# Kernel tuning notes

Hardware: AMD Instinct MI355X
Metric: run time of the kernel (lower is better)

Reference implementation:

```python
import jax, jax.numpy as jnp
import numpy as np

TEMPERATURE = 1.0
EPS = 1e-5
COS_EPS = 1e-8  # torch CosineSimilarity default eps
N_POS, N_NEG, D = 512, 512, 512


def setup_inputs() -> dict:
    key = jax.random.key(0)
    k1, k2, k3 = jax.random.split(key, 3)
    tensor_positive = jax.random.normal(k1, (N_POS, D), dtype=jnp.float32)
    tensor_negative = jax.random.normal(k2, (N_NEG, D), dtype=jnp.float32)
    # nn.Linear(512*3, 1), weight ~ N(0, 0.02^2), bias zeros
    linear_w = jax.random.normal(k3, (1, 3 * D), dtype=jnp.float32) * 0.02
    linear_b = jnp.zeros((1,), dtype=jnp.float32)
    return {"tensor_positive": tensor_positive, "tensor_negative": tensor_negative,
            "linear_w": linear_w, "linear_b": linear_b}


def _cos_matrix(a, b):
    # pairwise cosine similarity [Na, Nb], matching torch CosineSimilarity eps clamp
    an = a / jnp.maximum(jnp.linalg.norm(a, axis=-1, keepdims=True), COS_EPS)
    bn = b / jnp.maximum(jnp.linalg.norm(b, axis=-1, keepdims=True), COS_EPS)
    return an @ bn.T


def reference(tensor_positive, tensor_negative, linear_w, linear_b):
    pos, neg = tensor_positive, tensor_negative
    n_pos, d = pos.shape
    n_neg = neg.shape[0]

    # NCE part
    logit_n = jnp.exp(_cos_matrix(pos, neg) / TEMPERATURE)        # [N, M]
    deno_n = jnp.sum(logit_n, axis=-1)                            # [N]
    logit_p = jnp.exp(_cos_matrix(pos, pos) / TEMPERATURE)        # [N, N]
    loss = jnp.sum(-jnp.log(logit_p / (deno_n[:, None] + logit_p + EPS)))

    # Pairwise classifier: linear(cat([a, b, |a-b|])) decomposed as
    # a@w1 + b@w2 + |a-b|@w3 to avoid materializing the 3D concat.
    w = linear_w[0]
    w1, w2, w3 = w[:d], w[d:2 * d], w[2 * d:]
    allv = jnp.concatenate([pos, neg], axis=0)                    # [N+M, D]
    t1 = pos @ w1                                                 # [N]
    t2 = allv @ w2                                                # [N+M]
    diff = jnp.abs(pos[:, None, :] - allv[None, :, :])            # [N, N+M, D]
    t3 = jnp.einsum('nmd,d->nm', diff, w3)                        # [N, N+M]
    logits = t1[:, None] + t2[None, :] + t3 + linear_b[0]
    labels = jnp.concatenate([jnp.ones((n_pos,), jnp.float32),
                              jnp.zeros((n_neg,), jnp.float32)])  # [N+M]
    # BCE(sigmoid(logits), labels), stable form; per-i mean then sum over i
    bce = labels[None, :] * jax.nn.softplus(-logits) + (1.0 - labels[None, :]) * jax.nn.softplus(logits)
    loss = loss + jnp.sum(jnp.mean(bce, axis=1))
    return loss
```

## Files before the change

### kernel.cpp

```cpp
#include <hip/hip_runtime.h>
#include <math.h>

#define NPOS 512
#define DIM  512
#define NB   1024
#define EPSV 1e-5f
#define COS_EPS 1e-8f

#define OFF_INV  0
#define OFF_T1   1024
#define OFF_T2   1536
#define OFF_DENO 2560
#define OFF_COS  3072

__device__ __forceinline__ float softplus_f(float x) {
    return fmaxf(x, 0.f) + __logf(1.f + __expf(-fabsf(x)));
}

__global__ __launch_bounds__(256) void prep_kernel(
    const float* __restrict__ pos, const float* __restrict__ neg,
    const float* __restrict__ w, float* __restrict__ ws, float* __restrict__ out)
{
    int gtid = blockIdx.x * 256 + threadIdx.x;
    if (gtid == 0) out[0] = 0.f;
    if (gtid < NPOS) ws[OFF_DENO + gtid] = 0.f;
    int row  = gtid >> 6;
    int lane = threadIdx.x & 63;
    if (row >= NB) return;
    bool is_pos = row < NPOS;
    const float* r = is_pos ? pos + row * DIM : neg + (row - NPOS) * DIM;

    const float4* r4  = (const float4*)r + lane * 2;
    const float4* w14 = (const float4*)(w) + lane * 2;
    const float4* w24 = (const float4*)(w + DIM) + lane * 2;
    float4 a0 = r4[0],  a1 = r4[1];
    float4 u0 = w14[0], u1 = w14[1];
    float4 v0 = w24[0], v1 = w24[1];

    float ss  = a0.x*a0.x + a0.y*a0.y + a0.z*a0.z + a0.w*a0.w
              + a1.x*a1.x + a1.y*a1.y + a1.z*a1.z + a1.w*a1.w;
    float dw1 = a0.x*u0.x + a0.y*u0.y + a0.z*u0.z + a0.w*u0.w
              + a1.x*u1.x + a1.y*u1.y + a1.z*u1.z + a1.w*u1.w;
    float dw2 = a0.x*v0.x + a0.y*v0.y + a0.z*v0.z + a0.w*v0.w
              + a1.x*v1.x + a1.y*v1.y + a1.z*v1.z + a1.w*v1.w;

    #pragma unroll
    for (int off = 32; off; off >>= 1) {
        ss  += __shfl_xor(ss, off);
        dw1 += __shfl_xor(dw1, off);
        dw2 += __shfl_xor(dw2, off);
    }
    if (lane == 0) {
        float inv = 1.f / fmaxf(sqrtf(ss), COS_EPS);
        ws[OFF_INV + row] = inv;
        ws[OFF_T2 + row]  = dw2;
        if (is_pos) ws[OFF_T1 + row] = dw1;
    }
}

__global__ __launch_bounds__(256) void fused_kernel(
    const float* __restrict__ pos, const float* __restrict__ neg,
    const float* __restrict__ w, const float* __restrict__ lb,
    float* __restrict__ ws, float* __restrict__ out)
{
    __shared__ __align__(16) float As[2][32][36];
    __shared__ __align__(16) float Bs[2][32][36];
    __shared__ float red[4];

    const int tid = threadIdx.x;
    const int n0 = blockIdx.y * 32;
    const int m0 = blockIdx.x * 32;
    const bool isneg = (m0 >= NPOS);
    const float* Asrc = pos + (size_t)n0 * DIM;
    const float* Bsrc = isneg ? (neg + (size_t)(m0 - NPOS) * DIM)
                              : (pos + (size_t)m0 * DIM);
    const float* w3 = w + 2 * DIM;

    const int lr = tid >> 3;
    const int lc = (tid & 7) << 2;
    const int ti = tid >> 4;
    const int tj = tid & 15;

    float c[2][2] = {{0.f}}, t[2][2] = {{0.f}};

    float4 a0 = *(const float4*)(Asrc + lr * DIM + lc);
    float4 b0 = *(const float4*)(Bsrc + lr * DIM + lc);
    *(float4*)&As[0][lr][lc] = a0;
    *(float4*)&Bs[0][lr][lc] = b0;
    __syncthreads();

    #pragma unroll 1
    for (int iter = 0; iter < DIM / 32; ++iter) {
        const int cur = iter & 1;
        const bool more = (iter < DIM / 32 - 1);
        if (more) {
            const float* ap = Asrc + (iter + 1) * 32;
            const float* bp = Bsrc + (iter + 1) * 32;
            a0 = *(const float4*)(ap + lr * DIM + lc);
            b0 = *(const float4*)(bp + lr * DIM + lc);
        }
        const float* w3i = w3 + iter * 32;
        #pragma unroll
        for (int k = 0; k < 32; k += 4) {
            float4 av0 = *(const float4*)&As[cur][ti][k];
            float4 av1 = *(const float4*)&As[cur][ti + 16][k];
            float4 bv0 = *(const float4*)&Bs[cur][tj][k];
            float4 bv1 = *(const float4*)&Bs[cur][tj + 16][k];
            const float4 wv = *(const float4*)(w3i + k);
            #define ACC(r, s, AV, BV) \
                c[r][s] = fmaf(AV.x, BV.x, c[r][s]); \
                c[r][s] = fmaf(AV.y, BV.y, c[r][s]); \
                c[r][s] = fmaf(AV.z, BV.z, c[r][s]); \
                c[r][s] = fmaf(AV.w, BV.w, c[r][s]); \
                t[r][s] = fmaf(fabsf(AV.x - BV.x), wv.x, t[r][s]); \
                t[r][s] = fmaf(fabsf(AV.y - BV.y), wv.y, t[r][s]); \
                t[r][s] = fmaf(fabsf(AV.z - BV.z), wv.z, t[r][s]); \
                t[r][s] = fmaf(fabsf(AV.w - BV.w), wv.w, t[r][s]);
            ACC(0, 0, av0, bv0)
            ACC(0, 1, av0, bv1)
            ACC(1, 0, av1, bv0)
            ACC(1, 1, av1, bv1)
            #undef ACC
        }
        if (more) {
            *(float4*)&As[cur ^ 1][lr][lc] = a0;
            *(float4*)&Bs[cur ^ 1][lr][lc] = b0;
            __syncthreads();
        }
    }

    const float bias = lb[0];
    float inv_n[2], t1_n[2], inv_m[2], t2_m[2];
    #pragma unroll
    for (int r = 0; r < 2; ++r) {
        int n = n0 + ti + 16 * r;
        inv_n[r] = ws[OFF_INV + n];
        t1_n[r]  = ws[OFF_T1 + n];
    }
    #pragma unroll
    for (int s = 0; s < 2; ++s) {
        int m = m0 + tj + 16 * s;
        inv_m[s] = ws[OFF_INV + m];
        t2_m[s]  = ws[OFF_T2 + m];
    }

    float bce = 0.f;
    float rowsum[2] = {0.f, 0.f};
    #pragma unroll
    for (int r = 0; r < 2; ++r) {
        #pragma unroll
        for (int s = 0; s < 2; ++s) {
            float cc = c[r][s] * inv_n[r] * inv_m[s];
            float lg = t1_n[r] + t2_m[s] + t[r][s] + bias;
            bce += softplus_f(isneg ? lg : -lg);
            if (isneg) {
                rowsum[r] += __expf(cc);
            } else {
                int n = n0 + ti + 16 * r;
                int m = m0 + tj + 16 * s;
                ws[OFF_COS + (size_t)n * NPOS + m] = cc;
            }
        }
    }

    if (isneg) {
        #pragma unroll
        for (int off = 1; off < 16; off <<= 1) {
            rowsum[0] += __shfl_xor(rowsum[0], off);
            rowsum[1] += __shfl_xor(rowsum[1], off);
        }
        if (tj == 0) {
            atomicAdd(&ws[OFF_DENO + n0 + ti], rowsum[0]);
            atomicAdd(&ws[OFF_DENO + n0 + ti + 16], rowsum[1]);
        }
    }

    #pragma unroll
    for (int off = 32; off; off >>= 1) bce += __shfl_xor(bce, off);
    const int lane = tid & 63, wid = tid >> 6;
    if (lane == 0) red[wid] = bce;
    __syncthreads();
    if (tid == 0)
        atomicAdd(out, (red[0] + red[1] + red[2] + red[3]) * (1.f / 1024.f));
}

__global__ __launch_bounds__(128) void finish_kernel(
    float* __restrict__ ws, float* __restrict__ out)
{
    const int n = blockIdx.x * 2 + (threadIdx.x >> 6);
    const int l = threadIdx.x & 63;
    const float4* C = (const float4*)(ws + OFF_COS + (size_t)n * NPOS);
    const float deno = ws[OFF_DENO + n];

    float part = 0.f;
    #pragma unroll
    for (int j = 0; j < 2; ++j) {
        float4 cc = C[l + 64 * j];
        part += __logf(deno + __expf(cc.x) + EPSV) - cc.x;
        part += __logf(deno + __expf(cc.y) + EPSV) - cc.y;
        part += __logf(deno + __expf(cc.z) + EPSV) - cc.z;
        part += __logf(deno + __expf(cc.w) + EPSV) - cc.w;
    }

    #pragma unroll
    for (int off = 32; off; off >>= 1) part += __shfl_xor(part, off);
    if (l == 0) atomicAdd(out, part);
}

extern "C" void kernel_launch(void* const* d_in, const int* in_sizes, int n_in,
                              void* d_out, int out_size, void* d_ws, size_t ws_size,
                              hipStream_t stream) {
    (void)in_sizes; (void)n_in; (void)out_size; (void)ws_size;
    const float* pos = (const float*)d_in[0];
    const float* neg = (const float*)d_in[1];
    const float* w   = (const float*)d_in[2];
    const float* lb  = (const float*)d_in[3];
    float* out = (float*)d_out;
    float* ws  = (float*)d_ws;

    prep_kernel<<<256, 256, 0, stream>>>(pos, neg, w, ws, out);
    fused_kernel<<<dim3(32, 16), 256, 0, stream>>>(pos, neg, w, lb, ws, out);
    finish_kernel<<<256, 128, 0, stream>>>(ws, out);
}
```

Measured before the change: 99.04 us.

## Fold norm/projection prep into main tile kernel and replace atomics with partial buffers

New measurement: 113.4 us. 1.15x slower.

```diff
diff --git a/kernel.cpp b/kernel.cpp
--- a/kernel.cpp
+++ b/kernel.cpp
@@ -7,84 +7,54 @@
 #define EPSV 1e-5f
 #define COS_EPS 1e-8f
 
-#define OFF_INV  0
-#define OFF_T1   1024
-#define OFF_T2   1536
-#define OFF_DENO 2560
-#define OFF_COS  3072
+#define OFF_COS   0
+#define OFF_DENOP (NPOS * NPOS)
+#define OFF_BCEP  (OFF_DENOP + 16 * NPOS)
 
 __device__ __forceinline__ float softplus_f(float x) {
     return fmaxf(x, 0.f) + __logf(1.f + __expf(-fabsf(x)));
 }
 
-__global__ __launch_bounds__(256) void prep_kernel(
-    const float* __restrict__ pos, const float* __restrict__ neg,
-    const float* __restrict__ w, float* __restrict__ ws, float* __restrict__ out)
-{
-    int gtid = blockIdx.x * 256 + threadIdx.x;
-    if (gtid == 0) out[0] = 0.f;
-    if (gtid < NPOS) ws[OFF_DENO + gtid] = 0.f;
-    int row  = gtid >> 6;
-    int lane = threadIdx.x & 63;
-    if (row >= NB) return;
-    bool is_pos = row < NPOS;
-    const float* r = is_pos ? pos + row * DIM : neg + (row - NPOS) * DIM;
-
-    const float4* r4  = (const float4*)r + lane * 2;
-    const float4* w14 = (const float4*)(w) + lane * 2;
-    const float4* w24 = (const float4*)(w + DIM) + lane * 2;
-    float4 a0 = r4[0],  a1 = r4[1];
-    float4 u0 = w14[0], u1 = w14[1];
-    float4 v0 = w24[0], v1 = w24[1];
-
-    float ss  = a0.x*a0.x + a0.y*a0.y + a0.z*a0.z + a0.w*a0.w
-              + a1.x*a1.x + a1.y*a1.y + a1.z*a1.z + a1.w*a1.w;
-    float dw1 = a0.x*u0.x + a0.y*u0.y + a0.z*u0.z + a0.w*u0.w
-              + a1.x*u1.x + a1.y*u1.y + a1.z*u1.z + a1.w*u1.w;
-    float dw2 = a0.x*v0.x + a0.y*v0.y + a0.z*v0.z + a0.w*v0.w
-              + a1.x*v1.x + a1.y*v1.y + a1.z*v1.z + a1.w*v1.w;
-
-    #pragma unroll
-    for (int off = 32; off; off >>= 1) {
-        ss  += __shfl_xor(ss, off);
-        dw1 += __shfl_xor(dw1, off);
-        dw2 += __shfl_xor(dw2, off);
-    }
-    if (lane == 0) {
-        float inv = 1.f / fmaxf(sqrtf(ss), COS_EPS);
-        ws[OFF_INV + row] = inv;
-        ws[OFF_T2 + row]  = dw2;
-        if (is_pos) ws[OFF_T1 + row] = dw1;
-    }
-}
-
-__global__ __launch_bounds__(256) void fused_kernel(
+__device__ __forceinline__ float dot4(float4 a, float4 b) {
+    return a.x * b.x + a.y * b.y + a.z * b.z + a.w * b.w;
+}
+
+__global__ __launch_bounds__(256) void mega_kernel(
     const float* __restrict__ pos, const float* __restrict__ neg,
     const float* __restrict__ w, const float* __restrict__ lb,
     float* __restrict__ ws, float* __restrict__ out)
 {
     __shared__ __align__(16) float As[2][32][36];
     __shared__ __align__(16) float Bs[2][32][36];
+    __shared__ float smInvA[32], smT1A[32], smInvB[32], smT2B[32];
     __shared__ float red[4];
 
     const int tid = threadIdx.x;
     const int n0 = blockIdx.y * 32;
     const int m0 = blockIdx.x * 32;
+    const int bid = blockIdx.y * 32 + blockIdx.x;
     const bool isneg = (m0 >= NPOS);
     const float* Asrc = pos + (size_t)n0 * DIM;
     const float* Bsrc = isneg ? (neg + (size_t)(m0 - NPOS) * DIM)
                               : (pos + (size_t)m0 * DIM);
     const float* w3 = w + 2 * DIM;
 
+    if (bid == 0 && tid == 0) out[0] = 0.f;
+
     const int lr = tid >> 3;
     const int lc = (tid & 7) << 2;
     const int ti = tid >> 4;
     const int tj = tid & 15;
 
     float c[2][2] = {{0.f}}, t[2][2] = {{0.f}};
+    float ssa = 0.f, ssb = 0.f, t1a = 0.f, t2b = 0.f;
 
     float4 a0 = *(const float4*)(Asrc + lr * DIM + lc);
     float4 b0 = *(const float4*)(Bsrc + lr * DIM + lc);
+    float4 w1c = *(const float4*)(w + lc);
+    float4 w2c = *(const float4*)(w + DIM + lc);
+    ssa += dot4(a0, a0);  t1a += dot4(a0, w1c);
+    ssb += dot4(b0, b0);  t2b += dot4(b0, w2c);
     *(float4*)&As[0][lr][lc] = a0;
     *(float4*)&Bs[0][lr][lc] = b0;
     __syncthreads();
@@ -96,8 +66,10 @@
         if (more) {
             const float* ap = Asrc + (iter + 1) * 32;
             const float* bp = Bsrc + (iter + 1) * 32;
-            a0 = *(const float4*)(ap + lr * DIM + lc);
-            b0 = *(const float4*)(bp + lr * DIM + lc);
+            a0  = *(const float4*)(ap + lr * DIM + lc);
+            b0  = *(const float4*)(bp + lr * DIM + lc);
+            w1c = *(const float4*)(w + (iter + 1) * 32 + lc);
+            w2c = *(const float4*)(w + DIM + (iter + 1) * 32 + lc);
         }
         const float* w3i = w3 + iter * 32;
         #pragma unroll
@@ -123,25 +95,40 @@
             #undef ACC
         }
         if (more) {
+            ssa += dot4(a0, a0);  t1a += dot4(a0, w1c);
+            ssb += dot4(b0, b0);  t2b += dot4(b0, w2c);
             *(float4*)&As[cur ^ 1][lr][lc] = a0;
             *(float4*)&Bs[cur ^ 1][lr][lc] = b0;
             __syncthreads();
         }
     }
 
+    #pragma unroll
+    for (int off = 1; off < 8; off <<= 1) {
+        ssa += __shfl_xor(ssa, off);
+        t1a += __shfl_xor(t1a, off);
+        ssb += __shfl_xor(ssb, off);
+        t2b += __shfl_xor(t2b, off);
+    }
+    if ((tid & 7) == 0) {
+        smInvA[lr] = 1.f / fmaxf(sqrtf(ssa), COS_EPS);
+        smT1A[lr]  = t1a;
+        smInvB[lr] = 1.f / fmaxf(sqrtf(ssb), COS_EPS);
+        smT2B[lr]  = t2b;
+    }
+    __syncthreads();
+
     const float bias = lb[0];
     float inv_n[2], t1_n[2], inv_m[2], t2_m[2];
     #pragma unroll
     for (int r = 0; r < 2; ++r) {
-        int n = n0 + ti + 16 * r;
-        inv_n[r] = ws[OFF_INV + n];
-        t1_n[r]  = ws[OFF_T1 + n];
+        inv_n[r] = smInvA[ti + 16 * r];
+        t1_n[r]  = smT1A[ti + 16 * r];
     }
     #pragma unroll
     for (int s = 0; s < 2; ++s) {
-        int m = m0 + tj + 16 * s;
-        inv_m[s] = ws[OFF_INV + m];
-        t2_m[s]  = ws[OFF_T2 + m];
+        inv_m[s] = smInvB[tj + 16 * s];
+        t2_m[s]  = smT2B[tj + 16 * s];
     }
 
     float bce = 0.f;
@@ -169,9 +156,10 @@
             rowsum[0] += __shfl_xor(rowsum[0], off);
             rowsum[1] += __shfl_xor(rowsum[1], off);
         }
+        const int mb = blockIdx.x - 16;
         if (tj == 0) {
-            atomicAdd(&ws[OFF_DENO + n0 + ti], rowsum[0]);
-            atomicAdd(&ws[OFF_DENO + n0 + ti + 16], rowsum[1]);
+            ws[OFF_DENOP + mb * NPOS + n0 + ti]      = rowsum[0];
+            ws[OFF_DENOP + mb * NPOS + n0 + ti + 16] = rowsum[1];
         }
     }
 
@@ -181,30 +169,34 @@
     if (lane == 0) red[wid] = bce;
     __syncthreads();
     if (tid == 0)
-        atomicAdd(out, (red[0] + red[1] + red[2] + red[3]) * (1.f / 1024.f));
-}
-
-__global__ __launch_bounds__(128) void finish_kernel(
+        ws[OFF_BCEP + bid] = red[0] + red[1] + red[2] + red[3];
+}
+
+__global__ __launch_bounds__(256) void finish_kernel(
     float* __restrict__ ws, float* __restrict__ out)
 {
-    const int n = blockIdx.x * 2 + (threadIdx.x >> 6);
-    const int l = threadIdx.x & 63;
-    const float4* C = (const float4*)(ws + OFF_COS + (size_t)n * NPOS);
-    const float deno = ws[OFF_DENO + n];
-
-    float part = 0.f;
-    #pragma unroll
-    for (int j = 0; j < 2; ++j) {
-        float4 cc = C[l + 64 * j];
-        part += __logf(deno + __expf(cc.x) + EPSV) - cc.x;
-        part += __logf(deno + __expf(cc.y) + EPSV) - cc.y;
-        part += __logf(deno + __expf(cc.z) + EPSV) - cc.z;
-        part += __logf(deno + __expf(cc.w) + EPSV) - cc.w;
-    }
+    const int tid = threadIdx.x;
+    const int n = blockIdx.x * 2 + (tid >> 7);
+    const int tcol = tid & 127;
+    const int lane = tid & 63;
+
+    float dn = ws[OFF_DENOP + (lane & 15) * NPOS + n];
+    #pragma unroll
+    for (int off = 1; off < 16; off <<= 1) dn += __shfl_xor(dn, off);
+
+    float4 cc = *(const float4*)(ws + OFF_COS + (size_t)n * NPOS + 4 * tcol);
+    float part = __logf(dn + __expf(cc.x) + EPSV) - cc.x
+               + __logf(dn + __expf(cc.y) + EPSV) - cc.y
+               + __logf(dn + __expf(cc.z) + EPSV) - cc.z
+               + __logf(dn + __expf(cc.w) + EPSV) - cc.w;
+
+    if (tid == 0)
+        part += (ws[OFF_BCEP + 2 * blockIdx.x] + ws[OFF_BCEP + 2 * blockIdx.x + 1])
+                * (1.f / 1024.f);
 
     #pragma unroll
     for (int off = 32; off; off >>= 1) part += __shfl_xor(part, off);
-    if (l == 0) atomicAdd(out, part);
+    if (lane == 0) atomicAdd(out, part);
 }
 
 extern "C" void kernel_launch(void* const* d_in, const int* in_sizes, int n_in,
@@ -218,7 +210,6 @@
     float* out = (float*)d_out;
     float* ws  = (float*)d_ws;
 
-    prep_kernel<<<256, 256, 0, stream>>>(pos, neg, w, ws, out);
-    fused_kernel<<<dim3(32, 16), 256, 0, stream>>>(pos, neg, w, lb, ws, out);
-    finish_kernel<<<256, 128, 0, stream>>>(ws, out);
-}
+    mega_kernel<<<dim3(32, 16), 256, 0, stream>>>(pos, neg, w, lb, ws, out);
+    finish_kernel<<<256, 256, 0, stream>>>(ws, out);
+}
```

## Halve fused tile width to double block count and replace atomics with partial buffers

Applied to the files above, without the earlier changes.

After: 106.6 us. +7.7%, slower.

```diff
diff --git a/kernel.cpp b/kernel.cpp
--- a/kernel.cpp
+++ b/kernel.cpp
@@ -7,11 +7,12 @@
 #define EPSV 1e-5f
 #define COS_EPS 1e-8f
 
-#define OFF_INV  0
-#define OFF_T1   1024
-#define OFF_T2   1536
-#define OFF_DENO 2560
-#define OFF_COS  3072
+#define OFF_COS   0
+#define OFF_DENOP (NPOS * NPOS)
+#define OFF_BCEP  (OFF_DENOP + 32 * NPOS)
+#define OFF_INV   (OFF_BCEP + 1024)
+#define OFF_T1    (OFF_INV + NB)
+#define OFF_T2    (OFF_T1 + NPOS)
 
 __device__ __forceinline__ float softplus_f(float x) {
     return fmaxf(x, 0.f) + __logf(1.f + __expf(-fabsf(x)));
@@ -23,7 +24,6 @@
 {
     int gtid = blockIdx.x * 256 + threadIdx.x;
     if (gtid == 0) out[0] = 0.f;
-    if (gtid < NPOS) ws[OFF_DENO + gtid] = 0.f;
     int row  = gtid >> 6;
     int lane = threadIdx.x & 63;
     if (row >= NB) return;
@@ -58,35 +58,40 @@
     }
 }
 
-__global__ __launch_bounds__(256) void fused_kernel(
+__global__ __launch_bounds__(128) void fused_kernel(
     const float* __restrict__ pos, const float* __restrict__ neg,
     const float* __restrict__ w, const float* __restrict__ lb,
-    float* __restrict__ ws, float* __restrict__ out)
+    float* __restrict__ ws)
 {
     __shared__ __align__(16) float As[2][32][36];
-    __shared__ __align__(16) float Bs[2][32][36];
-    __shared__ float red[4];
+    __shared__ __align__(16) float Bs[2][16][20];
+    __shared__ float red[2];
 
     const int tid = threadIdx.x;
     const int n0 = blockIdx.y * 32;
-    const int m0 = blockIdx.x * 32;
+    const int m0 = blockIdx.x * 16;
+    const int bid = blockIdx.y * 64 + blockIdx.x;
     const bool isneg = (m0 >= NPOS);
     const float* Asrc = pos + (size_t)n0 * DIM;
     const float* Bsrc = isneg ? (neg + (size_t)(m0 - NPOS) * DIM)
                               : (pos + (size_t)m0 * DIM);
     const float* w3 = w + 2 * DIM;
 
-    const int lr = tid >> 3;
-    const int lc = (tid & 7) << 2;
-    const int ti = tid >> 4;
-    const int tj = tid & 15;
+    const int lrA = tid >> 2;
+    const int lcA = (tid & 3) << 3;
+    const int lrB = tid >> 3;
+    const int lcB = (tid & 7) << 2;
+    const int ti = tid >> 3;
+    const int tj = tid & 7;
 
     float c[2][2] = {{0.f}}, t[2][2] = {{0.f}};
 
-    float4 a0 = *(const float4*)(Asrc + lr * DIM + lc);
-    float4 b0 = *(const float4*)(Bsrc + lr * DIM + lc);
-    *(float4*)&As[0][lr][lc] = a0;
-    *(float4*)&Bs[0][lr][lc] = b0;
+    float4 a0 = *(const float4*)(Asrc + lrA * DIM + lcA);
+    float4 a1 = *(const float4*)(Asrc + lrA * DIM + lcA + 4);
+    float4 b0 = *(const float4*)(Bsrc + lrB * DIM + lcB);
+    *(float4*)&As[0][lrA][lcA]     = a0;
+    *(float4*)&As[0][lrA][lcA + 4] = a1;
+    *(float4*)&Bs[0][lrB][lcB]     = b0;
     __syncthreads();
 
     #pragma unroll 1
@@ -96,8 +101,9 @@
         if (more) {
             const float* ap = Asrc + (iter + 1) * 32;
             const float* bp = Bsrc + (iter + 1) * 32;
-            a0 = *(const float4*)(ap + lr * DIM + lc);
-            b0 = *(const float4*)(bp + lr * DIM + lc);
+            a0 = *(const float4*)(ap + lrA * DIM + lcA);
+            a1 = *(const float4*)(ap + lrA * DIM + lcA + 4);
+            b0 = *(const float4*)(bp + lrB * DIM + lcB);
         }
         const float* w3i = w3 + iter * 32;
         #pragma unroll
@@ -105,7 +111,7 @@
             float4 av0 = *(const float4*)&As[cur][ti][k];
             float4 av1 = *(const float4*)&As[cur][ti + 16][k];
             float4 bv0 = *(const float4*)&Bs[cur][tj][k];
-            float4 bv1 = *(const float4*)&Bs[cur][tj + 16][k];
+            float4 bv1 = *(const float4*)&Bs[cur][tj + 8][k];
             const float4 wv = *(const float4*)(w3i + k);
             #define ACC(r, s, AV, BV) \
                 c[r][s] = fmaf(AV.x, BV.x, c[r][s]); \
@@ -123,8 +129,9 @@
             #undef ACC
         }
         if (more) {
-            *(float4*)&As[cur ^ 1][lr][lc] = a0;
-            *(float4*)&Bs[cur ^ 1][lr][lc] = b0;
+            *(float4*)&As[cur ^ 1][lrA][lcA]     = a0;
+            *(float4*)&As[cur ^ 1][lrA][lcA + 4] = a1;
+            *(float4*)&Bs[cur ^ 1][lrB][lcB]     = b0;
             __syncthreads();
         }
     }
@@ -139,7 +146,7 @@
     }
     #pragma unroll
     for (int s = 0; s < 2; ++s) {
-        int m = m0 + tj + 16 * s;
+        int m = m0 + tj + 8 * s;
         inv_m[s] = ws[OFF_INV + m];
         t2_m[s]  = ws[OFF_T2 + m];
     }
@@ -157,7 +164,7 @@
                 rowsum[r] += __expf(cc);
             } else {
                 int n = n0 + ti + 16 * r;
-                int m = m0 + tj + 16 * s;
+                int m = m0 + tj + 8 * s;
                 ws[OFF_COS + (size_t)n * NPOS + m] = cc;
             }
         }
@@ -165,13 +172,14 @@
 
     if (isneg) {
         #pragma unroll
-        for (int off = 1; off < 16; off <<= 1) {
+        for (int off = 1; off < 8; off <<= 1) {
             rowsum[0] += __shfl_xor(rowsum[0], off);
             rowsum[1] += __shfl_xor(rowsum[1], off);
         }
+        const int mb = blockIdx.x - 32;
         if (tj == 0) {
-            atomicAdd(&ws[OFF_DENO + n0 + ti], rowsum[0]);
-            atomicAdd(&ws[OFF_DENO + n0 + ti + 16], rowsum[1]);
+            ws[OFF_DENOP + mb * NPOS + n0 + ti]      = rowsum[0];
+            ws[OFF_DENOP + mb * NPOS + n0 + ti + 16] = rowsum[1];
         }
     }
 
@@ -180,31 +188,35 @@
     const int lane = tid & 63, wid = tid >> 6;
     if (lane == 0) red[wid] = bce;
     __syncthreads();
-    if (tid == 0)
-        atomicAdd(out, (red[0] + red[1] + red[2] + red[3]) * (1.f / 1024.f));
-}
-
-__global__ __launch_bounds__(128) void finish_kernel(
+    if (tid == 0) ws[OFF_BCEP + bid] = red[0] + red[1];
+}
+
+__global__ __launch_bounds__(256) void finish_kernel(
     float* __restrict__ ws, float* __restrict__ out)
 {
-    const int n = blockIdx.x * 2 + (threadIdx.x >> 6);
-    const int l = threadIdx.x & 63;
-    const float4* C = (const float4*)(ws + OFF_COS + (size_t)n * NPOS);
-    const float deno = ws[OFF_DENO + n];
-
-    float part = 0.f;
-    #pragma unroll
-    for (int j = 0; j < 2; ++j) {
-        float4 cc = C[l + 64 * j];
-        part += __logf(deno + __expf(cc.x) + EPSV) - cc.x;
-        part += __logf(deno + __expf(cc.y) + EPSV) - cc.y;
-        part += __logf(deno + __expf(cc.z) + EPSV) - cc.z;
-        part += __logf(deno + __expf(cc.w) + EPSV) - cc.w;
+    const int tid = threadIdx.x;
+    const int n = blockIdx.x * 2 + (tid >> 7);
+    const int tcol = tid & 127;
+    const int lane = tid & 63;
+
+    float dn = ws[OFF_DENOP + (lane & 31) * NPOS + n];
+    #pragma unroll
+    for (int off = 1; off < 32; off <<= 1) dn += __shfl_xor(dn, off);
+
+    float4 cc = *(const float4*)(ws + OFF_COS + (size_t)n * NPOS + 4 * tcol);
+    float part = __logf(dn + __expf(cc.x) + EPSV) - cc.x
+               + __logf(dn + __expf(cc.y) + EPSV) - cc.y
+               + __logf(dn + __expf(cc.z) + EPSV) - cc.z
+               + __logf(dn + __expf(cc.w) + EPSV) - cc.w;
+
+    if (tid == 0) {
+        const float* bp = ws + OFF_BCEP + 4 * blockIdx.x;
+        part += (bp[0] + bp[1] + bp[2] + bp[3]) * (1.f / 1024.f);
     }
 
     #pragma unroll
     for (int off = 32; off; off >>= 1) part += __shfl_xor(part, off);
-    if (l == 0) atomicAdd(out, part);
+    if (lane == 0) atomicAdd(out, part);
 }
 
 extern "C" void kernel_launch(void* const* d_in, const int* in_sizes, int n_in,
@@ -219,6 +231,6 @@
     float* ws  = (float*)d_ws;
 
     prep_kernel<<<256, 256, 0, stream>>>(pos, neg, w, ws, out);
-    fused_kernel<<<dim3(32, 16), 256, 0, stream>>>(pos, neg, w, lb, ws, out);
-    finish_kernel<<<256, 128, 0, stream>>>(ws, out);
-}
+    fused_kernel<<<dim3(64, 16), 128, 0, stream>>>(pos, neg, w, lb, ws);
+    finish_kernel<<<256, 256, 0, stream>>>(ws, out);
+}
```

## Merge three kernels into one cooperative kernel with grid-wide syncs

Applied to the files above, without the earlier changes.

Result: slower. 188.7 us (+90.5%).

```diff
diff --git a/kernel.cpp b/kernel.cpp
--- a/kernel.cpp
+++ b/kernel.cpp
@@ -1,5 +1,8 @@
 #include <hip/hip_runtime.h>
+#include <hip/hip_cooperative_groups.h>
 #include <math.h>
+
+namespace cg = cooperative_groups;
 
 #define NPOS 512
 #define DIM  512
@@ -15,6 +18,195 @@
 
 __device__ __forceinline__ float softplus_f(float x) {
     return fmaxf(x, 0.f) + __logf(1.f + __expf(-fabsf(x)));
+}
+
+__global__ __launch_bounds__(256, 2) void mega_kernel(
+    const float* __restrict__ pos, const float* __restrict__ neg,
+    const float* __restrict__ w, const float* __restrict__ lb,
+    float* __restrict__ ws, float* __restrict__ out)
+{
+    __shared__ __align__(16) float As[2][32][36];
+    __shared__ __align__(16) float Bs[2][32][36];
+    __shared__ float red[4];
+
+    cg::grid_group grid = cg::this_grid();
+
+    const int tid  = threadIdx.x;
+    const int bid  = blockIdx.y * 32 + blockIdx.x;
+    const int lane = tid & 63;
+    const int wv   = tid >> 6;
+
+    if (bid == 0 && tid == 0) out[0] = 0.f;
+    if (tid == 0) ws[OFF_DENO + bid] = 0.f;
+    if (wv < 2) {
+        const int row = bid * 2 + wv;
+        const bool is_pos = row < NPOS;
+        const float* r = is_pos ? pos + row * DIM : neg + (row - NPOS) * DIM;
+        const float4* r4  = (const float4*)r + lane * 2;
+        const float4* w14 = (const float4*)(w) + lane * 2;
+        const float4* w24 = (const float4*)(w + DIM) + lane * 2;
+        float4 a0 = r4[0],  a1 = r4[1];
+        float4 u0 = w14[0], u1 = w14[1];
+        float4 v0 = w24[0], v1 = w24[1];
+
+        float ss  = a0.x*a0.x + a0.y*a0.y + a0.z*a0.z + a0.w*a0.w
+                  + a1.x*a1.x + a1.y*a1.y + a1.z*a1.z + a1.w*a1.w;
+        float dw1 = a0.x*u0.x + a0.y*u0.y + a0.z*u0.z + a0.w*u0.w
+                  + a1.x*u1.x + a1.y*u1.y + a1.z*u1.z + a1.w*u1.w;
+        float dw2 = a0.x*v0.x + a0.y*v0.y + a0.z*v0.z + a0.w*v0.w
+                  + a1.x*v1.x + a1.y*v1.y + a1.z*v1.z + a1.w*v1.w;
+
+        #pragma unroll
+        for (int off = 32; off; off >>= 1) {
+            ss  += __shfl_xor(ss, off);
+            dw1 += __shfl_xor(dw1, off);
+            dw2 += __shfl_xor(dw2, off);
+        }
+        if (lane == 0) {
+            float inv = 1.f / fmaxf(sqrtf(ss), COS_EPS);
+            ws[OFF_INV + row] = inv;
+            ws[OFF_T2 + row]  = dw2;
+            if (is_pos) ws[OFF_T1 + row] = dw1;
+        }
+    }
+
+    grid.sync();
+
+    {
+        const int n0 = blockIdx.y * 32;
+        const int m0 = blockIdx.x * 32;
+        const bool isneg = (m0 >= NPOS);
+        const float* Asrc = pos + (size_t)n0 * DIM;
+        const float* Bsrc = isneg ? (neg + (size_t)(m0 - NPOS) * DIM)
+                                  : (pos + (size_t)m0 * DIM);
+        const float* w3 = w + 2 * DIM;
+
+        const int lr = tid >> 3;
+        const int lc = (tid & 7) << 2;
+        const int ti = tid >> 4;
+        const int tj = tid & 15;
+
+        float c[2][2] = {{0.f}}, t[2][2] = {{0.f}};
+
+        float4 a0 = *(const float4*)(Asrc + lr * DIM + lc);
+        float4 b0 = *(const float4*)(Bsrc + lr * DIM + lc);
+        *(float4*)&As[0][lr][lc] = a0;
+        *(float4*)&Bs[0][lr][lc] = b0;
+        __syncthreads();
+
+        #pragma unroll 1
+        for (int iter = 0; iter < DIM / 32; ++iter) {
+            const int cur = iter & 1;
+            const bool more = (iter < DIM / 32 - 1);
+            if (more) {
+                const float* ap = Asrc + (iter + 1) * 32;
+                const float* bp = Bsrc + (iter + 1) * 32;
+                a0 = *(const float4*)(ap + lr * DIM + lc);
+                b0 = *(const float4*)(bp + lr * DIM + lc);
+            }
+            const float* w3i = w3 + iter * 32;
+            #pragma unroll
+            for (int k = 0; k < 32; k += 4) {
+                float4 av0 = *(const float4*)&As[cur][ti][k];
+                float4 av1 = *(const float4*)&As[cur][ti + 16][k];
+                float4 bv0 = *(const float4*)&Bs[cur][tj][k];
+                float4 bv1 = *(const float4*)&Bs[cur][tj + 16][k];
+                const float4 wv4 = *(const float4*)(w3i + k);
+                #define ACC(r, s, AV, BV) \
+                    c[r][s] = fmaf(AV.x, BV.x, c[r][s]); \
+                    c[r][s] = fmaf(AV.y, BV.y, c[r][s]); \
+                    c[r][s] = fmaf(AV.z, BV.z, c[r][s]); \
+                    c[r][s] = fmaf(AV.w, BV.w, c[r][s]); \
+                    t[r][s] = fmaf(fabsf(AV.x - BV.x), wv4.x, t[r][s]); \
+                    t[r][s] = fmaf(fabsf(AV.y - BV.y), wv4.y, t[r][s]); \
+                    t[r][s] = fmaf(fabsf(AV.z - BV.z), wv4.z, t[r][s]); \
+                    t[r][s] = fmaf(fabsf(AV.w - BV.w), wv4.w, t[r][s]);
+                ACC(0, 0, av0, bv0)
+                ACC(0, 1, av0, bv1)
+                ACC(1, 0, av1, bv0)
+                ACC(1, 1, av1, bv1)
+                #undef ACC
+            }
+            if (more) {
+                *(float4*)&As[cur ^ 1][lr][lc] = a0;
+                *(float4*)&Bs[cur ^ 1][lr][lc] = b0;
+                __syncthreads();
+            }
+        }
+
+        const float bias = lb[0];
+        float inv_n[2], t1_n[2], inv_m[2], t2_m[2];
+        #pragma unroll
+        for (int r = 0; r < 2; ++r) {
+            int n = n0 + ti + 16 * r;
+            inv_n[r] = ws[OFF_INV + n];
+            t1_n[r]  = ws[OFF_T1 + n];
+        }
+        #pragma unroll
+        for (int s = 0; s < 2; ++s) {
+            int m = m0 + tj + 16 * s;
+            inv_m[s] = ws[OFF_INV + m];
+            t2_m[s]  = ws[OFF_T2 + m];
+        }
+
+        float bce = 0.f;
+        float rowsum[2] = {0.f, 0.f};
+        #pragma unroll
+        for (int r = 0; r < 2; ++r) {
+            #pragma unroll
+            for (int s = 0; s < 2; ++s) {
+                float cc = c[r][s] * inv_n[r] * inv_m[s];
+                float lg = t1_n[r] + t2_m[s] + t[r][s] + bias;
+                bce += softplus_f(isneg ? lg : -lg);
+                if (isneg) {
+                    rowsum[r] += __expf(cc);
+                } else {
+                    int n = n0 + ti + 16 * r;
+                    int m = m0 + tj + 16 * s;
+                    ws[OFF_COS + (size_t)n * NPOS + m] = cc;
+                }
+            }
+        }
+
+        if (isneg) {
+            #pragma unroll
+            for (int off = 1; off < 16; off <<= 1) {
+                rowsum[0] += __shfl_xor(rowsum[0], off);
+                rowsum[1] += __shfl_xor(rowsum[1], off);
+            }
+            if (tj == 0) {
+                atomicAdd(&ws[OFF_DENO + n0 + ti], rowsum[0]);
+                atomicAdd(&ws[OFF_DENO + n0 + ti + 16], rowsum[1]);
+            }
+        }
+
+        #pragma unroll
+        for (int off = 32; off; off >>= 1) bce += __shfl_xor(bce, off);
+        if (lane == 0) red[wv] = bce;
+        __syncthreads();
+        if (tid == 0)
+            atomicAdd(out, (red[0] + red[1] + red[2] + red[3]) * (1.f / 1024.f));
+    }
+
+    grid.sync();
+
+    {
+        const int n = bid;
+        float part = 0.f;
+        if (tid < 128) {
+            const float dn = ws[OFF_DENO + n];
+            float4 cc = *(const float4*)(ws + OFF_COS + (size_t)n * NPOS + 4 * tid);
+            part = __logf(dn + __expf(cc.x) + EPSV) - cc.x
+                 + __logf(dn + __expf(cc.y) + EPSV) - cc.y
+                 + __logf(dn + __expf(cc.z) + EPSV) - cc.z
+                 + __logf(dn + __expf(cc.w) + EPSV) - cc.w;
+        }
+        #pragma unroll
+        for (int off = 32; off; off >>= 1) part += __shfl_xor(part, off);
+        if (lane == 0) red[wv] = part;
+        __syncthreads();
+        if (tid == 0) atomicAdd(out, red[0] + red[1] + red[2] + red[3]);
+    }
 }
 
 __global__ __launch_bounds__(256) void prep_kernel(
@@ -106,16 +298,16 @@
             float4 av1 = *(const float4*)&As[cur][ti + 16][k];
             float4 bv0 = *(const float4*)&Bs[cur][tj][k];
             float4 bv1 = *(const float4*)&Bs[cur][tj + 16][k];
-            const float4 wv = *(const float4*)(w3i + k);
+            const float4 wv4 = *(const float4*)(w3i + k);
             #define ACC(r, s, AV, BV) \
                 c[r][s] = fmaf(AV.x, BV.x, c[r][s]); \
                 c[r][s] = fmaf(AV.y, BV.y, c[r][s]); \
                 c[r][s] = fmaf(AV.z, BV.z, c[r][s]); \
                 c[r][s] = fmaf(AV.w, BV.w, c[r][s]); \
-                t[r][s] = fmaf(fabsf(AV.x - BV.x), wv.x, t[r][s]); \
-                t[r][s] = fmaf(fabsf(AV.y - BV.y), wv.y, t[r][s]); \
-                t[r][s] = fmaf(fabsf(AV.z - BV.z), wv.z, t[r][s]); \
-                t[r][s] = fmaf(fabsf(AV.w - BV.w), wv.w, t[r][s]);
+                t[r][s] = fmaf(fabsf(AV.x - BV.x), wv4.x, t[r][s]); \
+                t[r][s] = fmaf(fabsf(AV.y - BV.y), wv4.y, t[r][s]); \
+                t[r][s] = fmaf(fabsf(AV.z - BV.z), wv4.z, t[r][s]); \
+                t[r][s] = fmaf(fabsf(AV.w - BV.w), wv4.w, t[r][s]);
             ACC(0, 0, av0, bv0)
             ACC(0, 1, av0, bv1)
             ACC(1, 0, av1, bv0)
@@ -218,7 +410,14 @@
     float* out = (float*)d_out;
     float* ws  = (float*)d_ws;
 
-    prep_kernel<<<256, 256, 0, stream>>>(pos, neg, w, ws, out);
-    fused_kernel<<<dim3(32, 16), 256, 0, stream>>>(pos, neg, w, lb, ws, out);
-    finish_kernel<<<256, 128, 0, stream>>>(ws, out);
-}
+    void* args[] = {(void*)&pos, (void*)&neg, (void*)&w, (void*)&lb,
+                    (void*)&ws, (void*)&out};
+    hipError_t err = hipLaunchCooperativeKernel((const void*)mega_kernel,
+                                                dim3(32, 16), dim3(256),
+                                                args, 0, stream);
+    if (err != hipSuccess) {
+        prep_kernel<<<256, 256, 0, stream>>>(pos, neg, w, ws, out);
+        fused_kernel<<<dim3(32, 16), 256, 0, stream>>>(pos, neg, w, lb, ws, out);
+        finish_kernel<<<256, 128, 0, stream>>>(ws, out);
+    }
+}
```
